# Kernel tuning notes

Measured on AMD Instinct MI355X. Metric: run time of the kernel, lower is better.

Reference implementation:

```python
import jax, jax.numpy as jnp
import numpy as np

WS = 7        # window_size
SHIFT = 3     # shift_size
NH = 3        # num_heads
E = 96        # embed_dim
B, H, W = 8, 224, 224


def _relative_position_index(ws: int) -> np.ndarray:
    coords = np.stack(np.meshgrid(np.arange(ws), np.arange(ws), indexing='ij')).reshape(2, -1)
    rel = coords[:, :, None] - coords[:, None, :]          # (2, N, N)
    rel = rel.transpose(1, 2, 0) + (ws - 1)                # (N, N, 2)
    rel[:, :, 0] *= 2 * ws - 1
    return rel.sum(-1)                                      # (N, N) in [0, (2ws-1)^2)


def setup_inputs() -> dict:
    key = jax.random.key(0)
    ks = jax.random.split(key, 6)
    x = jax.random.normal(ks[0], (B, H, W, E), dtype=jnp.float32)
    # nn.MultiheadAttention params: packed in_proj (3E,E)+(3E,), out_proj (E,E)+(E,)
    w_qkv = jax.random.normal(ks[1], (3 * E, E), dtype=jnp.float32) * 0.02
    b_qkv = jax.random.normal(ks[2], (3 * E,), dtype=jnp.float32) * 0.02
    w_out = jax.random.normal(ks[3], (E, E), dtype=jnp.float32) * 0.02
    b_out = jax.random.normal(ks[4], (E,), dtype=jnp.float32) * 0.02
    bias_table = jax.random.normal(ks[5], ((2 * WS - 1) ** 2, NH), dtype=jnp.float32) * 0.02
    rel_index = jnp.asarray(_relative_position_index(WS), dtype=jnp.int32)
    return {"x": x, "w_qkv": w_qkv, "b_qkv": b_qkv, "w_out": w_out,
            "b_out": b_out, "bias_table": bias_table, "rel_index": rel_index}


def reference(x, w_qkv, b_qkv, w_out, b_out, bias_table, rel_index):
    ws, shift = WS, SHIFT
    Bq, Hq, Wq, C = x.shape
    nh = bias_table.shape[-1]
    hd = C // nh
    N = ws * ws

    # cyclic shift
    xs = jnp.roll(x, (-shift, -shift), axis=(1, 2))

    Hp = -(-Hq // ws) * ws
    Wp = -(-Wq // ws) * ws
    xs = jnp.pad(xs, ((0, 0), (0, Hp - Hq), (0, Wp - Wq), (0, 0)))

    # window partition -> (B*nW, N, C)
    win = xs.reshape(Bq, Hp // ws, ws, Wp // ws, ws, C)
    win = win.transpose(0, 1, 3, 2, 4, 5).reshape(-1, N, C)

    # packed QKV projection (torch Linear: x @ W.T + b)
    qkv = win @ w_qkv.T + b_qkv
    q, k, v = jnp.split(qkv, 3, axis=-1)
    hsplit = lambda t: t.reshape(t.shape[0], N, nh, hd)
    q, k, v = hsplit(q), hsplit(k), hsplit(v)

    # scaled attention scores + relative position bias (used as attn_mask in torch)
    scale = 1.0 / jnp.sqrt(jnp.asarray(hd, dtype=q.dtype))
    scores = jnp.einsum('bnhd,bmhd->bhnm', q * scale, k)    # (B*nW, h, N, N)
    bias = bias_table[rel_index].transpose(2, 0, 1)         # (h, N, N)
    attn = jax.nn.softmax(scores + bias[None], axis=-1)

    out = jnp.einsum('bhnm,bmhd->bnhd', attn, v).reshape(-1, N, C)
    out = out @ w_out.T + b_out

    # window reverse + crop + reverse shift
    out = out.reshape(Bq, Hp // ws, Wp // ws, ws, ws, C)
    out = out.transpose(0, 1, 3, 2, 4, 5).reshape(Bq, Hp, Wp, C)[:, :Hq, :Wq, :]
    return jnp.roll(out, (shift, shift), axis=(1, 2))
```

## Files before the change

### kernel.cpp

```cpp
#include <hip/hip_runtime.h>
#include <cstddef>


typedef _Float16 half8 __attribute__((ext_vector_type(8)));
typedef float f4v __attribute__((ext_vector_type(4)));
typedef unsigned short u16;
typedef unsigned int u32;

#define MFMA(A, B, C) __builtin_amdgcn_mfma_f32_16x16x32_f16((A), (B), (C), 0, 0, 0)

__device__ inline u16 f16b(float f) { return __builtin_bit_cast(u16, (_Float16)f); }
__device__ inline u32 pkrtz(float a, float b) {
    return __builtin_bit_cast(u32, __builtin_amdgcn_cvt_pkrtz(a, b));
}
__device__ inline int SWU(int a, int kg) {
    return (((a ^ (kg << 1) ^ ((a & 8) >> 1)) & 15) | (kg << 4));
}

__global__ void prep_kernel(const float* __restrict__ wqkv, const float* __restrict__ wout,
                            const float* __restrict__ btab, const int* __restrict__ ridx,
                            u16* __restrict__ wq16, u16* __restrict__ wo16,
                            float* __restrict__ bmat)
{
    const int i = blockIdx.x * 256 + threadIdx.x;
    if (i < 27648) {
        wq16[i] = f16b(wqkv[i]);
    } else if (i < 36864) {
        wo16[i - 27648] = f16b(wout[i - 27648]);
    } else if (i < 36864 + 12288) {
        const int j = i - 36864;
        const int h = j >> 12, rem = j & 4095;
        const int r = rem >> 6, u = rem & 63;
        bmat[j] = (r < 49 && u < 49) ? btab[ridx[r * 49 + u] * 3 + h] : 0.f;
    }
}

__global__ __launch_bounds__(256, 4)
void swin_kernel(const float* __restrict__ x,
                 const u16* __restrict__ wq16,
                 const u16* __restrict__ wo16,
                 const float* __restrict__ bqkv,
                 const float* __restrict__ bout,
                 const float* __restrict__ bm,
                 float* __restrict__ out)
{
    __shared__ __attribute__((aligned(16))) char smem[40960];
    constexpr int QT = 0, KT = 12288, VT = 24576, PL = 36864;

    const int tid  = threadIdx.x;
    const int w    = tid >> 6;
    const int lane = tid & 63;
    const int l15  = lane & 15;
    const int lg   = lane >> 4;

    const int blk = blockIdx.x;
    const int bb  = blk >> 10;
    const int wi7 = ((blk >> 5) & 31) * 7;
    const int wj7 = (blk & 31) * 7;

    const float SCALE = 0.17677669529663688f;
    const int swbase = SWU(l15, lg) * 16;

    half8 xa[4][3];
    #pragma unroll
    for (int m = 0; m < 4; ++m) {
        const int t = m * 16 + l15;
        if (t < 49) {
            const int tr = t / 7, tc = t - tr * 7;
            int r = wi7 + tr + 3; if (r >= 224) r -= 224;
            int c = wj7 + tc + 3; if (c >= 224) c -= 224;
            const float* xrow = x + ((size_t)((bb * 224 + r) * 224 + c)) * 96 + lg * 8;
            #pragma unroll
            for (int ks = 0; ks < 3; ++ks) {
                const float4 f0 = *(const float4*)(xrow + ks * 32);
                const float4 f1 = *(const float4*)(xrow + ks * 32 + 4);
                uint4 pk;
                pk.x = pkrtz(f0.x, f0.y); pk.y = pkrtz(f0.z, f0.w);
                pk.z = pkrtz(f1.x, f1.y); pk.w = pkrtz(f1.z, f1.w);
                xa[m][ks] = __builtin_bit_cast(half8, pk);
            }
        } else {
            const uint4 z = {0, 0, 0, 0};
            xa[m][0] = xa[m][1] = xa[m][2] = __builtin_bit_cast(half8, z);
        }
    }

    {
        const int sw1 = ((lg >> 1) & 1) * 4;
        half8 bcur[3], bnxt[3];
        int n = w;
        {
            const u16* bp = wq16 + (size_t)(n * 16 + l15) * 96 + lg * 8;
            bcur[0] = *(const half8*)(bp);
            bcur[1] = *(const half8*)(bp + 32);
            bcur[2] = *(const half8*)(bp + 64);
        }
        while (true) {
            const int n2 = n + 4;
            if (n2 < 18) {
                const u16* bp = wq16 + (size_t)(n2 * 16 + l15) * 96 + lg * 8;
                bnxt[0] = *(const half8*)(bp);
                bnxt[1] = *(const half8*)(bp + 32);
                bnxt[2] = *(const half8*)(bp + 64);
            }
            f4v acc[4];
            #pragma unroll
            for (int m = 0; m < 4; ++m) {
                f4v a = {0.f, 0.f, 0.f, 0.f};
                a = MFMA(xa[m][0], bcur[0], a);
                a = MFMA(xa[m][1], bcur[1], a);
                a = MFMA(xa[m][2], bcur[2], a);
                acc[m] = a;
            }
            const int oc = n * 16 + l15;
            const float bias = bqkv[oc];
            if (n < 12) {
                const int c  = (n < 6) ? oc : oc - 96;
                const int hh = c >> 5, d = c & 31;
                const int kg = d >> 3, el = d & 7;
                const float mul = (n < 6) ? SCALE : 1.0f;
                char* reg0 = smem + ((n < 6) ? QT : KT) + (hh * 4) * 1024 + el * 2;
                const int xr = (kg << 1) ^ sw1;
                #pragma unroll
                for (int m = 0; m < 4; ++m) {
                    #pragma unroll
                    for (int i = 0; i < 4; ++i) {
                        const float v = (acc[m][i] + bias) * mul;
                        const int unit = (((lg * 4 + i) ^ xr) & 15) | (kg << 4);
                        *(u16*)(reg0 + m * 1024 + unit * 16) = f16b(v);
                    }
                }
            } else {
                const int c  = oc - 192;
                const int hh = c >> 5, nd = (c >> 4) & 1;
                const int elb = (lg & 1) * 4;
                #pragma unroll
                for (int m = 0; m < 4; ++m) {
                    const int ku = m >> 1;
                    const int kg = (m & 1) * 2 + (lg >> 1);
                    uint2 pv;
                    pv.x = pkrtz(acc[m][0] + bias, acc[m][1] + bias);
                    pv.y = pkrtz(acc[m][2] + bias, acc[m][3] + bias);
                    *(uint2*)(smem + VT + ((hh * 2 + nd) * 2 + ku) * 1024 +
                              SWU(l15, kg) * 16 + elb * 2) = pv;
                }
            }
            if (n2 >= 18) break;
            bcur[0] = bnxt[0]; bcur[1] = bnxt[1]; bcur[2] = bnxt[2];
            n = n2;
        }
    }
    __syncthreads();

    {
        const int t = w * 16 + l15;
        const int elb2 = ((lg & 1) * 4) * 2;
        for (int h = 0; h < 3; ++h) {
            const int qfr = QT + (h * 4 + w) * 1024;
            const half8 qa = *(const half8*)(smem + qfr + swbase);
            f4v s[4];
            #pragma unroll
            for (int ut = 0; ut < 4; ++ut) {
                const half8 kb = *(const half8*)(smem + KT + (h * 4 + ut) * 1024 + swbase);
                f4v z = {0.f, 0.f, 0.f, 0.f};
                s[ut] = MFMA(kb, qa, z);
            }
            const float* bp = bm + h * 4096 + t * 64 + lg * 4;
            #pragma unroll
            for (int ut = 0; ut < 4; ++ut) {
                const float4 bv = *(const float4*)(bp + ut * 16);
                s[ut][0] += bv.x; s[ut][1] += bv.y; s[ut][2] += bv.z; s[ut][3] += bv.w;
            }
            s[3][1] = -1e30f; s[3][2] = -1e30f; s[3][3] = -1e30f;
            if (lg) s[3][0] = -1e30f;
            float mx = -1e30f;
            #pragma unroll
            for (int ut = 0; ut < 4; ++ut)
                #pragma unroll
                for (int i = 0; i < 4; ++i) mx = fmaxf(mx, s[ut][i]);
            mx = fmaxf(mx, __shfl_xor(mx, 16));
            mx = fmaxf(mx, __shfl_xor(mx, 32));
            float sm = 0.f;
            #pragma unroll
            for (int ut = 0; ut < 4; ++ut)
                #pragma unroll
                for (int i = 0; i < 4; ++i) { const float e = __expf(s[ut][i] - mx); s[ut][i] = e; sm += e; }
            sm += __shfl_xor(sm, 16);
            sm += __shfl_xor(sm, 32);
            const float inv = 1.f / sm;
            #pragma unroll
            for (int ut = 0; ut < 4; ++ut) {
                uint2 pv;
                pv.x = pkrtz(s[ut][0] * inv, s[ut][1] * inv);
                pv.y = pkrtz(s[ut][2] * inv, s[ut][3] * inv);
                const int kg = (ut & 1) * 2 + (lg >> 1);
                const int base = (ut < 2) ? qfr : (PL + w * 1024);
                *(uint2*)(smem + base + SWU(l15, kg) * 16 + elb2) = pv;
            }
            const half8 p0 = *(const half8*)(smem + qfr + swbase);
            const half8 p1 = *(const half8*)(smem + PL + w * 1024 + swbase);
            #pragma unroll
            for (int nd = 0; nd < 2; ++nd) {
                f4v o = {0.f, 0.f, 0.f, 0.f};
                o = MFMA(*(const half8*)(smem + VT + ((h * 2 + nd) * 2 + 0) * 1024 + swbase), p0, o);
                o = MFMA(*(const half8*)(smem + VT + ((h * 2 + nd) * 2 + 1) * 1024 + swbase), p1, o);
                uint2 ov;
                ov.x = pkrtz(o[0], o[1]);
                ov.y = pkrtz(o[2], o[3]);
                const int kg = nd * 2 + (lg >> 1);
                *(uint2*)(smem + qfr + SWU(l15, kg) * 16 + elb2) = ov;
            }
        }
    }
    __syncthreads();

    {
        #pragma unroll
        for (int q = 0; q < 6; ++q) {
            const int p = w * 6 + q;
            const int nn = p >> 2, m = p & 3;
            f4v acc = {0.f, 0.f, 0.f, 0.f};
            #pragma unroll
            for (int ks = 0; ks < 3; ++ks) {
                const half8 wa = *(const half8*)(wo16 + (size_t)(nn * 16 + l15) * 96 + ks * 32 + lg * 8);
                const half8 ob = *(const half8*)(smem + QT + (ks * 4 + m) * 1024 + swbase);
                acc = MFMA(wa, ob, acc);
            }
            const int t = m * 16 + l15;
            if (t < 49) {
                const int tr = t / 7, tc = t - tr * 7;
                int r = wi7 + tr + 3; if (r >= 224) r -= 224;
                int c = wj7 + tc + 3; if (c >= 224) c -= 224;
                const float4 bo = *(const float4*)(bout + nn * 16 + lg * 4);
                float4 res;
                res.x = acc[0] + bo.x; res.y = acc[1] + bo.y;
                res.z = acc[2] + bo.z; res.w = acc[3] + bo.w;
                *(float4*)(out + ((size_t)((bb * 224 + r) * 224 + c)) * 96 + nn * 16 + lg * 4) = res;
            }
        }
    }
}

extern "C" void kernel_launch(void* const* d_in, const int* in_sizes, int n_in,
                              void* d_out, int out_size, void* d_ws, size_t ws_size,
                              hipStream_t stream) {
    const float* x          = (const float*)d_in[0];
    const float* w_qkv      = (const float*)d_in[1];
    const float* b_qkv      = (const float*)d_in[2];
    const float* w_out      = (const float*)d_in[3];
    const float* b_out      = (const float*)d_in[4];
    const float* bias_table = (const float*)d_in[5];
    const int*   rel_index  = (const int*)d_in[6];
    float* outp = (float*)d_out;

    u16* wq16 = (u16*)d_ws;
    u16* wo16 = wq16 + 27648;
    float* bmat = (float*)((char*)d_ws + 73728);

    prep_kernel<<<dim3(192), dim3(256), 0, stream>>>(
        w_qkv, w_out, bias_table, rel_index, wq16, wo16, bmat);
    swin_kernel<<<dim3(8192), dim3(256), 0, stream>>>(
        x, wq16, wo16, b_qkv, b_out, bmat, outp);
}
```

Baseline: 201.7 us.

## Restructure QKV projection per-wave token tiles, fold scale and log2e into weights

```diff
diff --git a/kernel.cpp b/kernel.cpp
--- a/kernel.cpp
+++ b/kernel.cpp
@@ -19,19 +19,27 @@
 
 __global__ void prep_kernel(const float* __restrict__ wqkv, const float* __restrict__ wout,
                             const float* __restrict__ btab, const int* __restrict__ ridx,
+                            const float* __restrict__ bqkv,
                             u16* __restrict__ wq16, u16* __restrict__ wo16,
-                            float* __restrict__ bmat)
+                            float* __restrict__ bmat, float* __restrict__ bqs)
 {
     const int i = blockIdx.x * 256 + threadIdx.x;
+    const float QS = 0.17677669529663688f * 1.4426950408889634f;
     if (i < 27648) {
-        wq16[i] = f16b(wqkv[i]);
+        float f = wqkv[i];
+        if (i < 9216) f *= QS;
+        wq16[i] = f16b(f);
     } else if (i < 36864) {
         wo16[i - 27648] = f16b(wout[i - 27648]);
-    } else if (i < 36864 + 12288) {
+    } else if (i < 49152) {
         const int j = i - 36864;
-        const int h = j >> 12, rem = j & 4095;
-        const int r = rem >> 6, u = rem & 63;
-        bmat[j] = (r < 49 && u < 49) ? btab[ridx[r * 49 + u] * 3 + h] : 0.f;
+        const int h = j >> 12, rem = j & 4095, r = rem >> 6, u = rem & 63;
+        bmat[j] = (r < 49 && u < 49) ? btab[ridx[r * 49 + u] * 3 + h] * 1.4426950408889634f : 0.f;
+    } else if (i < 49440) {
+        const int j = i - 49152;
+        float f = bqkv[j];
+        if (j < 96) f *= QS;
+        bqs[j] = f;
     }
 }
 
@@ -39,7 +47,7 @@
 void swin_kernel(const float* __restrict__ x,
                  const u16* __restrict__ wq16,
                  const u16* __restrict__ wo16,
-                 const float* __restrict__ bqkv,
+                 const float* __restrict__ bqs,
                  const float* __restrict__ bout,
                  const float* __restrict__ bm,
                  float* __restrict__ out)
@@ -58,112 +66,101 @@
     const int wi7 = ((blk >> 5) & 31) * 7;
     const int wj7 = (blk & 31) * 7;
 
-    const float SCALE = 0.17677669529663688f;
     const int swbase = SWU(l15, lg) * 16;
-
-    half8 xa[4][3];
-    #pragma unroll
-    for (int m = 0; m < 4; ++m) {
-        const int t = m * 16 + l15;
-        if (t < 49) {
-            const int tr = t / 7, tc = t - tr * 7;
-            int r = wi7 + tr + 3; if (r >= 224) r -= 224;
-            int c = wj7 + tc + 3; if (c >= 224) c -= 224;
-            const float* xrow = x + ((size_t)((bb * 224 + r) * 224 + c)) * 96 + lg * 8;
-            #pragma unroll
-            for (int ks = 0; ks < 3; ++ks) {
-                const float4 f0 = *(const float4*)(xrow + ks * 32);
-                const float4 f1 = *(const float4*)(xrow + ks * 32 + 4);
-                uint4 pk;
-                pk.x = pkrtz(f0.x, f0.y); pk.y = pkrtz(f0.z, f0.w);
-                pk.z = pkrtz(f1.x, f1.y); pk.w = pkrtz(f1.z, f1.w);
-                xa[m][ks] = __builtin_bit_cast(half8, pk);
-            }
-        } else {
-            const uint4 z = {0, 0, 0, 0};
-            xa[m][0] = xa[m][1] = xa[m][2] = __builtin_bit_cast(half8, z);
-        }
-    }
-
-    {
-        const int sw1 = ((lg >> 1) & 1) * 4;
-        half8 bcur[3], bnxt[3];
-        int n = w;
-        {
-            const u16* bp = wq16 + (size_t)(n * 16 + l15) * 96 + lg * 8;
-            bcur[0] = *(const half8*)(bp);
-            bcur[1] = *(const half8*)(bp + 32);
-            bcur[2] = *(const half8*)(bp + 64);
-        }
-        while (true) {
-            const int n2 = n + 4;
-            if (n2 < 18) {
-                const u16* bp = wq16 + (size_t)(n2 * 16 + l15) * 96 + lg * 8;
-                bnxt[0] = *(const half8*)(bp);
-                bnxt[1] = *(const half8*)(bp + 32);
-                bnxt[2] = *(const half8*)(bp + 64);
-            }
-            f4v acc[4];
-            #pragma unroll
-            for (int m = 0; m < 4; ++m) {
-                f4v a = {0.f, 0.f, 0.f, 0.f};
-                a = MFMA(xa[m][0], bcur[0], a);
-                a = MFMA(xa[m][1], bcur[1], a);
-                a = MFMA(xa[m][2], bcur[2], a);
-                acc[m] = a;
-            }
-            const int oc = n * 16 + l15;
-            const float bias = bqkv[oc];
+    const int elb    = ((lg & 1) * 4) * 2;
+
+    half8 xb[3];
+    {
+        const int t = w * 16 + l15;
+        const int tr = t / 7, tc = t - tr * 7;
+        int r = wi7 + tr + 3; if (r >= 224) r -= 224;
+        int c = wj7 + tc + 3; if (c >= 224) c -= 224;
+        const float* xrow = x + ((size_t)((bb * 224 + r) * 224 + c)) * 96 + lg * 8;
+        #pragma unroll
+        for (int ks = 0; ks < 3; ++ks) {
+            const float4 f0 = *(const float4*)(xrow + ks * 32);
+            const float4 f1 = *(const float4*)(xrow + ks * 32 + 4);
+            uint4 pk;
+            pk.x = pkrtz(f0.x, f0.y); pk.y = pkrtz(f0.z, f0.w);
+            pk.z = pkrtz(f1.x, f1.y); pk.w = pkrtz(f1.z, f1.w);
+            xb[ks] = __builtin_bit_cast(half8, pk);
+        }
+    }
+    {
+        const u16* wbase = wq16 + (size_t)l15 * 96 + lg * 8;
+        half8 wf[3][3];
+        #pragma unroll
+        for (int s3 = 0; s3 < 3; ++s3) {
+            const u16* p = wbase + s3 * 1536;
+            wf[s3][0] = *(const half8*)(p);
+            wf[s3][1] = *(const half8*)(p + 32);
+            wf[s3][2] = *(const half8*)(p + 64);
+        }
+        #pragma unroll
+        for (int n = 0; n < 18; ++n) {
+            const int cs = n % 3;
+            f4v acc = {0.f, 0.f, 0.f, 0.f};
             if (n < 12) {
-                const int c  = (n < 6) ? oc : oc - 96;
-                const int hh = c >> 5, d = c & 31;
-                const int kg = d >> 3, el = d & 7;
-                const float mul = (n < 6) ? SCALE : 1.0f;
-                char* reg0 = smem + ((n < 6) ? QT : KT) + (hh * 4) * 1024 + el * 2;
-                const int xr = (kg << 1) ^ sw1;
-                #pragma unroll
-                for (int m = 0; m < 4; ++m) {
-                    #pragma unroll
-                    for (int i = 0; i < 4; ++i) {
-                        const float v = (acc[m][i] + bias) * mul;
-                        const int unit = (((lg * 4 + i) ^ xr) & 15) | (kg << 4);
-                        *(u16*)(reg0 + m * 1024 + unit * 16) = f16b(v);
-                    }
-                }
+                acc = MFMA(wf[cs][0], xb[0], acc);
+                acc = MFMA(wf[cs][1], xb[1], acc);
+                acc = MFMA(wf[cs][2], xb[2], acc);
             } else {
-                const int c  = oc - 192;
-                const int hh = c >> 5, nd = (c >> 4) & 1;
-                const int elb = (lg & 1) * 4;
-                #pragma unroll
-                for (int m = 0; m < 4; ++m) {
-                    const int ku = m >> 1;
-                    const int kg = (m & 1) * 2 + (lg >> 1);
-                    uint2 pv;
-                    pv.x = pkrtz(acc[m][0] + bias, acc[m][1] + bias);
-                    pv.y = pkrtz(acc[m][2] + bias, acc[m][3] + bias);
-                    *(uint2*)(smem + VT + ((hh * 2 + nd) * 2 + ku) * 1024 +
-                              SWU(l15, kg) * 16 + elb * 2) = pv;
-                }
-            }
-            if (n2 >= 18) break;
-            bcur[0] = bnxt[0]; bcur[1] = bnxt[1]; bcur[2] = bnxt[2];
-            n = n2;
+                acc = MFMA(xb[0], wf[cs][0], acc);
+                acc = MFMA(xb[1], wf[cs][1], acc);
+                acc = MFMA(xb[2], wf[cs][2], acc);
+            }
+            if (n < 15) {
+                const u16* p = wbase + (n + 3) * 1536;
+                wf[cs][0] = *(const half8*)(p);
+                wf[cs][1] = *(const half8*)(p + 32);
+                wf[cs][2] = *(const half8*)(p + 64);
+            }
+            if (n < 12) {
+                const float4 b4 = *(const float4*)(bqs + n * 16 + lg * 4);
+                uint2 pv;
+                pv.x = pkrtz(acc[0] + b4.x, acc[1] + b4.y);
+                pv.y = pkrtz(acc[2] + b4.z, acc[3] + b4.w);
+                char* dst = smem + ((n < 6) ? (QT + (((n >> 1) * 4 + w) << 10))
+                                            : (KT + ((((n - 6) >> 1) * 4 + w) << 10)));
+                const int kg = ((n & 1) << 1) + (lg >> 1);
+                *(uint2*)(dst + SWU(l15, kg) * 16 + elb) = pv;
+            } else {
+                const float bv = bqs[n * 16 + l15];
+                uint2 pv;
+                pv.x = pkrtz(acc[0] + bv, acc[1] + bv);
+                pv.y = pkrtz(acc[2] + bv, acc[3] + bv);
+                const int h = (n - 12) >> 1, nd = n & 1;
+                const int kg = ((w & 1) << 1) + (lg >> 1);
+                *(uint2*)(smem + VT + (((h * 2 + nd) * 2 + (w >> 1)) << 10) +
+                          SWU(l15, kg) * 16 + elb) = pv;
+            }
         }
     }
     __syncthreads();
 
     {
         const int t = w * 16 + l15;
-        const int elb2 = ((lg & 1) * 4) * 2;
+        half8 qa = *(const half8*)(smem + QT + ((0 * 4 + w) << 10) + swbase);
+        half8 kb[4];
+        #pragma unroll
+        for (int ut = 0; ut < 4; ++ut)
+            kb[ut] = *(const half8*)(smem + KT + ((0 * 4 + ut) << 10) + swbase);
+
+        #pragma unroll
         for (int h = 0; h < 3; ++h) {
-            const int qfr = QT + (h * 4 + w) * 1024;
-            const half8 qa = *(const half8*)(smem + qfr + swbase);
+            const int qfr = QT + ((h * 4 + w) << 10);
             f4v s[4];
             #pragma unroll
             for (int ut = 0; ut < 4; ++ut) {
-                const half8 kb = *(const half8*)(smem + KT + (h * 4 + ut) * 1024 + swbase);
                 f4v z = {0.f, 0.f, 0.f, 0.f};
-                s[ut] = MFMA(kb, qa, z);
+                s[ut] = MFMA(kb[ut], qa, z);
+            }
+            half8 qan; half8 kbn[4];
+            if (h < 2) {
+                qan = *(const half8*)(smem + QT + (((h + 1) * 4 + w) << 10) + swbase);
+                #pragma unroll
+                for (int ut = 0; ut < 4; ++ut)
+                    kbn[ut] = *(const half8*)(smem + KT + (((h + 1) * 4 + ut) << 10) + swbase);
             }
             const float* bp = bm + h * 4096 + t * 64 + lg * 4;
             #pragma unroll
@@ -184,7 +181,10 @@
             #pragma unroll
             for (int ut = 0; ut < 4; ++ut)
                 #pragma unroll
-                for (int i = 0; i < 4; ++i) { const float e = __expf(s[ut][i] - mx); s[ut][i] = e; sm += e; }
+                for (int i = 0; i < 4; ++i) {
+                    const float e = exp2f(s[ut][i] - mx);
+                    s[ut][i] = e; sm += e;
+                }
             sm += __shfl_xor(sm, 16);
             sm += __shfl_xor(sm, 32);
             const float inv = 1.f / sm;
@@ -194,21 +194,26 @@
                 pv.x = pkrtz(s[ut][0] * inv, s[ut][1] * inv);
                 pv.y = pkrtz(s[ut][2] * inv, s[ut][3] * inv);
                 const int kg = (ut & 1) * 2 + (lg >> 1);
-                const int base = (ut < 2) ? qfr : (PL + w * 1024);
-                *(uint2*)(smem + base + SWU(l15, kg) * 16 + elb2) = pv;
+                const int base = (ut < 2) ? qfr : (PL + (w << 10));
+                *(uint2*)(smem + base + SWU(l15, kg) * 16 + elb) = pv;
             }
             const half8 p0 = *(const half8*)(smem + qfr + swbase);
-            const half8 p1 = *(const half8*)(smem + PL + w * 1024 + swbase);
+            const half8 p1 = *(const half8*)(smem + PL + (w << 10) + swbase);
             #pragma unroll
             for (int nd = 0; nd < 2; ++nd) {
                 f4v o = {0.f, 0.f, 0.f, 0.f};
-                o = MFMA(*(const half8*)(smem + VT + ((h * 2 + nd) * 2 + 0) * 1024 + swbase), p0, o);
-                o = MFMA(*(const half8*)(smem + VT + ((h * 2 + nd) * 2 + 1) * 1024 + swbase), p1, o);
+                o = MFMA(*(const half8*)(smem + VT + (((h * 2 + nd) * 2 + 0) << 10) + swbase), p0, o);
+                o = MFMA(*(const half8*)(smem + VT + (((h * 2 + nd) * 2 + 1) << 10) + swbase), p1, o);
                 uint2 ov;
                 ov.x = pkrtz(o[0], o[1]);
                 ov.y = pkrtz(o[2], o[3]);
                 const int kg = nd * 2 + (lg >> 1);
-                *(uint2*)(smem + qfr + SWU(l15, kg) * 16 + elb2) = ov;
+                *(uint2*)(smem + qfr + SWU(l15, kg) * 16 + elb) = ov;
+            }
+            if (h < 2) {
+                qa = qan;
+                #pragma unroll
+                for (int ut = 0; ut < 4; ++ut) kb[ut] = kbn[ut];
             }
         }
     }
@@ -223,7 +228,7 @@
             #pragma unroll
             for (int ks = 0; ks < 3; ++ks) {
                 const half8 wa = *(const half8*)(wo16 + (size_t)(nn * 16 + l15) * 96 + ks * 32 + lg * 8);
-                const half8 ob = *(const half8*)(smem + QT + (ks * 4 + m) * 1024 + swbase);
+                const half8 ob = *(const half8*)(smem + QT + ((ks * 4 + m) << 10) + swbase);
                 acc = MFMA(wa, ob, acc);
             }
             const int t = m * 16 + l15;
@@ -256,9 +261,10 @@
     u16* wq16 = (u16*)d_ws;
     u16* wo16 = wq16 + 27648;
     float* bmat = (float*)((char*)d_ws + 73728);
-
-    prep_kernel<<<dim3(192), dim3(256), 0, stream>>>(
-        w_qkv, w_out, bias_table, rel_index, wq16, wo16, bmat);
+    float* bqs  = (float*)((char*)d_ws + 122880);
+
+    prep_kernel<<<dim3(194), dim3(256), 0, stream>>>(
+        w_qkv, w_out, bias_table, rel_index, b_qkv, wq16, wo16, bmat, bqs);
     swin_kernel<<<dim3(8192), dim3(256), 0, stream>>>(
-        x, wq16, wo16, b_qkv, b_out, bmat, outp);
-}
+        x, wq16, wo16, bqs, b_out, bmat, outp);
+}
```

Measured after the change: 271.6 us. 1.35x slower.
